# Kernel optimization log

Measured on AMD Instinct MI355X. Metric: run time of the kernel, lower is better.

## Reference

```python
import jax, jax.numpy as jnp
import numpy as np

B, L, ENC_IN, C_OUT = 8, 2048, 21, 21
D_MODEL, EXPAND, D_STATE, D_CONV = 512, 2, 16, 4
D_INNER = D_MODEL * EXPAND
DT_RANK = (D_MODEL + 15) // 16  # 'auto' => ceil(d_model/16) = 32
MARK_DIM = 4  # timeF features for freq='h'
PRED_LEN = 96


def setup_inputs() -> dict:
    key = jax.random.key(0)
    ks = jax.random.split(key, 13)
    s = 0.02
    return {
        'x_enc': jax.random.normal(ks[0], (B, L, ENC_IN), jnp.float32),
        'x_mark_enc': jax.random.normal(ks[1], (B, L, MARK_DIM), jnp.float32),
        'x_dec': jax.random.normal(ks[2], (B, PRED_LEN, ENC_IN), jnp.float32),
        'x_mark_dec': jax.random.normal(ks[3], (B, PRED_LEN, MARK_DIM), jnp.float32),
        'conv_w': jax.random.normal(ks[4], (D_MODEL, ENC_IN, 3), jnp.float32) * s,      # TokenEmbedding circular conv
        'temp_w': jax.random.normal(ks[5], (D_MODEL, MARK_DIM), jnp.float32) * s,       # TimeFeatureEmbedding (no bias)
        'in_proj_w': jax.random.normal(ks[6], (2 * D_INNER, D_MODEL), jnp.float32) * s,
        'conv1d_w': jax.random.normal(ks[7], (D_INNER, 1, D_CONV), jnp.float32) * s,    # depthwise causal conv
        'conv1d_b': jnp.zeros((D_INNER,), jnp.float32),
        'x_proj_w': jax.random.normal(ks[8], (DT_RANK + 2 * D_STATE, D_INNER), jnp.float32) * s,
        'dt_proj_w': jax.random.normal(ks[9], (D_INNER, DT_RANK), jnp.float32) * s,
        'dt_proj_b': jax.random.normal(ks[10], (D_INNER,), jnp.float32) * 0.1,
        'A_log': jnp.log(jnp.tile(jnp.arange(1, D_STATE + 1, dtype=jnp.float32), (D_INNER, 1))),  # mamba S4D-real init
        'D': jnp.ones((D_INNER,), jnp.float32),
        'out_proj_w': jax.random.normal(ks[11], (D_MODEL, D_INNER), jnp.float32) * s,
        'head_w': jax.random.normal(ks[12], (C_OUT, D_MODEL), jnp.float32) * s,
    }


def _pos_embedding(seq_len, d):
    pos = jnp.arange(seq_len, dtype=jnp.float32)[:, None]
    div = jnp.exp(jnp.arange(0, d, 2, dtype=jnp.float32) * (-np.log(10000.0) / d))
    pe = jnp.zeros((seq_len, d), jnp.float32)
    pe = pe.at[:, 0::2].set(jnp.sin(pos * div))
    pe = pe.at[:, 1::2].set(jnp.cos(pos * div))
    return pe


def _mamba(x, in_proj_w, conv1d_w, conv1d_b, x_proj_w, dt_proj_w, dt_proj_b, A_log, D):
    Bsz = x.shape[0]
    xz = x @ in_proj_w.T                          # (B,L,2*Din)
    xs, z = jnp.split(xz, 2, axis=-1)
    # causal depthwise conv1d over time (pad left d_conv-1, truncate to L)
    xc = jnp.pad(xs.transpose(0, 2, 1), ((0, 0), (0, 0), (D_CONV - 1, 0)))
    xc = jax.lax.conv_general_dilated(xc, conv1d_w, (1,), 'VALID',
                                      dimension_numbers=('NCH', 'OIH', 'NCH'),
                                      feature_group_count=D_INNER)
    xs = jax.nn.silu((xc + conv1d_b[None, :, None]).transpose(0, 2, 1))  # (B,L,Din)
    x_dbl = xs @ x_proj_w.T                       # (B,L,dt_rank+2N)
    dt, Bm, Cm = jnp.split(x_dbl, [DT_RANK, DT_RANK + D_STATE], axis=-1)
    delta = jax.nn.softplus(dt @ dt_proj_w.T + dt_proj_b)  # (B,L,Din)
    A = -jnp.exp(A_log)                           # (Din,N)

    def step(h, inp):
        u_t, d_t, b_t, c_t = inp                  # (B,Din),(B,Din),(B,N),(B,N)
        dA = jnp.exp(d_t[:, :, None] * A)         # (B,Din,N)
        h = dA * h + (d_t * u_t)[:, :, None] * b_t[:, None, :]
        return h, jnp.einsum('bdn,bn->bd', h, c_t)

    h0 = jnp.zeros((Bsz, D_INNER, D_STATE), xs.dtype)
    seq = (xs.transpose(1, 0, 2), delta.transpose(1, 0, 2),
           Bm.transpose(1, 0, 2), Cm.transpose(1, 0, 2))
    _, ys = jax.lax.scan(step, h0, seq)
    y = ys.transpose(1, 0, 2) + xs * D            # (B,L,Din)
    return y * jax.nn.silu(z)


def _forward(x_enc, x_mark_enc, conv_w, temp_w, in_proj_w, conv1d_w, conv1d_b,
             x_proj_w, dt_proj_w, dt_proj_b, A_log, D, out_proj_w, head_w):
    # RevIN-style instance norm over time (stats detached)
    mean = jax.lax.stop_gradient(jnp.mean(x_enc, axis=1, keepdims=True))
    xc = x_enc - mean
    std = jax.lax.stop_gradient(jnp.sqrt(jnp.var(xc, axis=1, keepdims=True) + 1e-5))
    xn = xc / std
    # TokenEmbedding: circular-padded conv1d, kernel 3, no bias
    xt = jnp.pad(xn.transpose(0, 2, 1), ((0, 0), (0, 0), (1, 1)), mode='wrap')
    val = jax.lax.conv_general_dilated(xt, conv_w, (1,), 'VALID',
                                       dimension_numbers=('NCH', 'OIH', 'NCH')).transpose(0, 2, 1)
    emb = val + x_mark_enc @ temp_w.T + _pos_embedding(x_enc.shape[1], D_MODEL)[None]
    y = _mamba(emb, in_proj_w, conv1d_w, conv1d_b, x_proj_w, dt_proj_w, dt_proj_b, A_log, D)
    y = y @ out_proj_w.T                          # Mamba out_proj (no bias)
    out = y @ head_w.T                            # final Linear (no bias)
    out = out * std + mean                        # de-normalize
    return out[:, -PRED_LEN:, :]


def reference(x_enc, x_mark_enc, x_dec, x_mark_dec, conv_w, temp_w, in_proj_w,
              conv1d_w, conv1d_b, x_proj_w, dt_proj_w, dt_proj_b, A_log, D,
              out_proj_w, head_w):
    # x_dec / x_mark_dec are accepted but unused by the forecast path
    return _forward(x_enc, x_mark_enc, conv_w, temp_w, in_proj_w, conv1d_w,
                    conv1d_b, x_proj_w, dt_proj_w, dt_proj_b, A_log, D,
                    out_proj_w, head_w)
```

## Files before the change

kernel.cpp:

```cpp
#include <hip/hip_runtime.h>
#include <hip/hip_bf16.h>
#include <math.h>

#define Bsz 8
#define Lseq 2048
#define ENC_IN 21
#define C_OUT 21
#define D_MODEL 512
#define D_INNER 1024
#define D_STATE 16
#define D_CONV 4
#define DT_RANK 32
#define MARK_DIM 4
#define PRED_LEN 96
#define L_TAIL (Lseq - PRED_LEN)
#define K_EMB 80
#define CHUNK 128
#define NCHUNK_A 15
#define MTOT (Bsz * Lseq)
#define PITCH (MTOT + 16)

#define PE_C0 (-9.210340371976184f / (float)D_MODEL)

typedef __attribute__((ext_vector_type(8))) short short8;
typedef __attribute__((ext_vector_type(4))) float f32x4;

__global__ void stats_kernel(const float* __restrict__ x_enc,
                             float* __restrict__ mean, float* __restrict__ stdv) {
    int bc = blockIdx.x;
    int b = bc / ENC_IN, c = bc % ENC_IN;
    __shared__ float red[256], red2[256];
    int t = threadIdx.x;
    float s = 0.f, s2 = 0.f;
    for (int l = t; l < Lseq; l += 256) {
        float x = x_enc[((size_t)b * Lseq + l) * ENC_IN + c];
        s += x; s2 += x * x;
    }
    red[t] = s; red2[t] = s2; __syncthreads();
    for (int off = 128; off > 0; off >>= 1) {
        if (t < off) { red[t] += red[t + off]; red2[t] += red2[t + off]; }
        __syncthreads();
    }
    if (t == 0) {
        float m = red[0] / (float)Lseq;
        float v = red2[0] / (float)Lseq - m * m;
        mean[bc] = m;
        stdv[bc] = sqrtf(fmaxf(v, 0.f) + 1e-5f);
    }
}

__global__ void fuse_w_kernel(const float* __restrict__ head_w,
                              const float* __restrict__ out_proj_w,
                              float* __restrict__ W) {
    int idx = blockIdx.x * 256 + threadIdx.x;
    if (idx >= C_OUT * D_INNER) return;
    int c = idx / D_INNER, d = idx % D_INNER;
    float s = 0.f;
    for (int k = 0; k < D_MODEL; ++k)
        s += head_w[c * D_MODEL + k] * out_proj_w[(size_t)k * D_INNER + d];
    W[idx] = s;
}

__global__ void prep_wT_kernel(const float* __restrict__ conv_w,
                               const float* __restrict__ temp_w,
                               float* __restrict__ WembT) {
    int idx = blockIdx.x * 256 + threadIdx.x;
    int k = idx / D_MODEL, d = idx % D_MODEL;
    float v = 0.f;
    if (k < 3 * ENC_IN) {
        int kk = k / ENC_IN, c = k % ENC_IN;
        v = conv_w[((size_t)d * ENC_IN + c) * 3 + kk];
    } else if (k < 3 * ENC_IN + MARK_DIM) {
        v = temp_w[d * MARK_DIM + (k - 3 * ENC_IN)];
    }
    WembT[idx] = v;
}

__global__ void prep_x_kernel(const float* __restrict__ x_enc,
                              const float* __restrict__ x_mark,
                              const float* __restrict__ mean,
                              const float* __restrict__ stdv,
                              float* __restrict__ xin) {
    int idx = blockIdx.x * 256 + threadIdx.x;
    int bl = idx / K_EMB, k = idx % K_EMB;
    int b = bl >> 11, l = bl & (Lseq - 1);
    float v = 0.f;
    if (k < 3 * ENC_IN) {
        int kk = k / ENC_IN, c = k % ENC_IN;
        int ll = (l + kk - 1 + Lseq) & (Lseq - 1);
        v = (x_enc[((size_t)b * Lseq + ll) * ENC_IN + c] - mean[b * ENC_IN + c])
            / stdv[b * ENC_IN + c];
    } else if (k < 3 * ENC_IN + MARK_DIM) {
        v = x_mark[((size_t)b * Lseq + l) * MARK_DIM + (k - 3 * ENC_IN)];
    }
    xin[idx] = v;
}

__global__ void wcomb_kernel(const float* __restrict__ in_proj_w,
                             const float* __restrict__ WembT,
                             float* __restrict__ Wcomb) {
    int idx = blockIdx.x * 256 + threadIdx.x;
    int j = idx / K_EMB, k = idx % K_EMB;
    const float* a = in_proj_w + (size_t)j * D_MODEL;
    const float* b = WembT + (size_t)k * D_MODEL;
    float s = 0.f;
    for (int d = 0; d < D_MODEL; d += 4) {
        float4 av = *(const float4*)(a + d);
        float4 bv = *(const float4*)(b + d);
        s += av.x * bv.x + av.y * bv.y + av.z * bv.z + av.w * bv.w;
    }
    Wcomb[idx] = s;
}

__global__ void pepz_kernel(const float* __restrict__ in_proj_w,
                            float* __restrict__ PEpZ) {
    __shared__ float per[D_MODEL];
    int lz = blockIdx.x;
    int q = blockIdx.y;
    int t = threadIdx.x;
    {
        int l = L_TAIL + lz;
        float div = __expf((float)(2 * t) * PE_C0);
        float s, c;
        sincosf((float)l * div, &s, &c);
        per[2 * t] = s;
        per[2 * t + 1] = c;
    }
    __syncthreads();
    int j = q * 256 + t;
    const float* w = in_proj_w + (size_t)(D_INNER + j) * D_MODEL;
    float s = 0.f;
    for (int d = 0; d < D_MODEL; d += 4) {
        float4 wv = *(const float4*)(w + d);
        s += per[d] * wv.x + per[d + 1] * wv.y + per[d + 2] * wv.z + per[d + 3] * wv.w;
    }
    PEpZ[(size_t)lz * D_INNER + j] = s;
}

template <int AMODE, int BMODE, int EPI>
__launch_bounds__(256)
__global__ void gemm(const float* __restrict__ A, const float* __restrict__ B,
                     float* __restrict__ C0, const float* __restrict__ bias,
                     int M, int N, int K, int lda, int ldb) {
    __shared__ float As[16][65];
    __shared__ float Bs[16][65];
    int bm = blockIdx.y, bn = blockIdx.x;
    int t = threadIdx.x;
    int tx = t & 15, ty = t >> 4;
    float acc[4][4] = {};
    int arow = bm * 64, bcol = bn * 64;
    int lr = t >> 2;
    int lk = (t & 3) * 4;

    size_t aRow;
    {
        int r = arow + lr;
        if (AMODE == 3) {
            int rb = r / PRED_LEN;
            int rl = r - rb * PRED_LEN;
            aRow = (size_t)rb * Lseq + L_TAIL + rl;
        } else {
            aRow = (size_t)r;
        }
    }

    for (int k0 = 0; k0 < K; k0 += 16) {
        {
            float4 av = *(const float4*)(A + aRow * lda + k0 + lk);
            As[lk + 0][lr] = av.x; As[lk + 1][lr] = av.y;
            As[lk + 2][lr] = av.z; As[lk + 3][lr] = av.w;
        }
        {
            float4 bv = *(const float4*)(B + (size_t)(bcol + lr) * ldb + k0 + lk);
            Bs[lk + 0][lr] = bv.x; Bs[lk + 1][lr] = bv.y;
            Bs[lk + 2][lr] = bv.z; Bs[lk + 3][lr] = bv.w;
        }
        __syncthreads();
        #pragma unroll
        for (int kk = 0; kk < 16; ++kk) {
            float a[4], bq[4];
            #pragma unroll
            for (int i = 0; i < 4; ++i) a[i] = As[kk][ty * 4 + i];
            #pragma unroll
            for (int j = 0; j < 4; ++j) bq[j] = Bs[kk][tx * 4 + j];
            #pragma unroll
            for (int i = 0; i < 4; ++i)
                #pragma unroll
                for (int j = 0; j < 4; ++j)
                    acc[i][j] += a[i] * bq[j];
        }
        __syncthreads();
    }

    #pragma unroll
    for (int i = 0; i < 4; ++i) {
        int row = arow + ty * 4 + i;
        #pragma unroll
        for (int j = 0; j < 4; ++j) {
            int col = bcol + tx * 4 + j;
            float v = acc[i][j];
            if (EPI == 3) {
                v += bias[(size_t)(row % PRED_LEN) * N + col];
            }
            C0[(size_t)row * N + col] = v;
        }
    }
}

__device__ __forceinline__ void split_bf16(float x, short& hb, short& lb) {
    unsigned u = __float_as_uint(x);
    unsigned short h = (unsigned short)(u >> 16);
    float hf = __uint_as_float(((unsigned)h) << 16);
    unsigned short l = (unsigned short)(__float_as_uint(x - hf) >> 16);
    hb = (short)h; lb = (short)l;
}

template <int BMODE, int EPI>
__launch_bounds__(256)
__global__ void mfma_gemm128(const float* __restrict__ A, const float* __restrict__ B,
                             float* __restrict__ C, const float* __restrict__ bias,
                             int M, int N, int K, int lda, int ldb, int ldc) {
    __shared__ short Ah[128][48], Al[128][48];
    __shared__ short Bh[64][48], Bl[64][48];
    int t = threadIdx.x;
    int bn0 = blockIdx.x * 64;
    int am0 = blockIdx.y * 128;
    int w = t >> 6, l = t & 63;
    int lr = l & 15, lk = l >> 4;

    f32x4 acc[2][4];
    #pragma unroll
    for (int i = 0; i < 2; ++i)
        #pragma unroll
        for (int j = 0; j < 4; ++j) acc[i][j] = (f32x4){0.f, 0.f, 0.f, 0.f};

    const int mst = t >> 2, kst = (t & 3) * 8;

    for (int kb = 0; kb < K; kb += 32) {
        if (kb) __syncthreads();
        #pragma unroll
        for (int half = 0; half < 2; ++half) {
            int m = mst + half * 64;
            const float* src = A + (size_t)(am0 + m) * lda + kb + kst;
            short8 hv, lv;
            if (kb + 32 <= K) {
                float4 a0 = *(const float4*)(src);
                float4 a1 = *(const float4*)(src + 4);
                float xs[8] = {a0.x, a0.y, a0.z, a0.w, a1.x, a1.y, a1.z, a1.w};
                #pragma unroll
                for (int j = 0; j < 8; ++j) {
                    short hb, lb; split_bf16(xs[j], hb, lb);
                    hv[j] = hb; lv[j] = lb;
                }
            } else {
                #pragma unroll
                for (int j = 0; j < 8; ++j) {
                    float x = (kb + kst + j < K) ? src[j] : 0.f;
                    short hb, lb; split_bf16(x, hb, lb);
                    hv[j] = hb; lv[j] = lb;
                }
            }
            *(short8*)&Ah[m][kst] = hv;
            *(short8*)&Al[m][kst] = lv;
        }
        if constexpr (BMODE == 0) {
            short8 hv, lv;
            #pragma unroll
            for (int j = 0; j < 8; ++j) {
                int k = kb + kst + j;
                float x = (k < K) ? B[(size_t)k * ldb + bn0 + mst] : 0.f;
                short hb, lb; split_bf16(x, hb, lb);
                hv[j] = hb; lv[j] = lb;
            }
            *(short8*)&Bh[mst][kst] = hv;
            *(short8*)&Bl[mst][kst] = lv;
        } else if constexpr (BMODE == 1) {
            float ng = (float)(bn0 + mst);
            short8 hv, lv;
            #pragma unroll
            for (int p = 0; p < 4; ++p) {
                float e = __expf((float)(kb + kst + 2 * p) * PE_C0);
                float sv, cv;
                sincosf(ng * e, &sv, &cv);
                short hb, lb;
                split_bf16(sv, hb, lb); hv[2 * p] = hb; lv[2 * p] = lb;
                split_bf16(cv, hb, lb); hv[2 * p + 1] = hb; lv[2 * p + 1] = lb;
            }
            *(short8*)&Bh[mst][kst] = hv;
            *(short8*)&Bl[mst][kst] = lv;
        } else {
            const float* src = B + (size_t)(bn0 + mst) * ldb + kb + kst;
            short8 hv, lv;
            if (kb + 32 <= K) {
                float4 b0 = *(const float4*)(src);
                float4 b1 = *(const float4*)(src + 4);
                float xs[8] = {b0.x, b0.y, b0.z, b0.w, b1.x, b1.y, b1.z, b1.w};
                #pragma unroll
                for (int j = 0; j < 8; ++j) {
                    short hb, lb; split_bf16(xs[j], hb, lb);
                    hv[j] = hb; lv[j] = lb;
                }
            } else {
                #pragma unroll
                for (int j = 0; j < 8; ++j) {
                    float x = (kb + kst + j < K) ? src[j] : 0.f;
                    short hb, lb; split_bf16(x, hb, lb);
                    hv[j] = hb; lv[j] = lb;
                }
            }
            *(short8*)&Bh[mst][kst] = hv;
            *(short8*)&Bl[mst][kst] = lv;
        }
        __syncthreads();
        #pragma unroll
        for (int mt = 0; mt < 2; ++mt) {
            short8 a_hi = *(const short8*)&Ah[mt * 64 + w * 16 + lr][lk * 8];
            short8 a_lo = *(const short8*)&Al[mt * 64 + w * 16 + lr][lk * 8];
            #pragma unroll
            for (int t4 = 0; t4 < 4; ++t4) {
                short8 b_hi = *(const short8*)&Bh[t4 * 16 + lr][lk * 8];
                short8 b_lo = *(const short8*)&Bl[t4 * 16 + lr][lk * 8];
                acc[mt][t4] = __builtin_amdgcn_mfma_f32_16x16x32_bf16(a_hi, b_hi, acc[mt][t4], 0, 0, 0);
                acc[mt][t4] = __builtin_amdgcn_mfma_f32_16x16x32_bf16(a_lo, b_hi, acc[mt][t4], 0, 0, 0);
                acc[mt][t4] = __builtin_amdgcn_mfma_f32_16x16x32_bf16(a_hi, b_lo, acc[mt][t4], 0, 0, 0);
            }
        }
    }

    #pragma unroll
    for (int mt = 0; mt < 2; ++mt) {
        #pragma unroll
        for (int t4 = 0; t4 < 4; ++t4) {
            #pragma unroll
            for (int r = 0; r < 4; ++r) {
                int row = am0 + mt * 64 + w * 16 + lk * 4 + r;
                int col = bn0 + t4 * 16 + lr;
                float v = acc[mt][t4][r];
                if (EPI == 1) {
                    v += bias[row];
                    v = (v > 20.f) ? v : log1pf(__expf(v));
                }
                if (EPI == 2) {
                    v += bias[(size_t)row * Lseq + (col & (Lseq - 1))];
                }
                C[(size_t)row * ldc + col] = v;
            }
        }
    }
}

template <int BMODE, int EPI>
__launch_bounds__(256)
__global__ void mfma_gemm64(const float* __restrict__ A, const float* __restrict__ B,
                            float* __restrict__ C, const float* __restrict__ bias,
                            int M, int N, int K, int lda, int ldb, int ldc) {
    __shared__ short Ah[64][48], Al[64][48];
    __shared__ short Bh[64][48], Bl[64][48];
    int t = threadIdx.x;
    int bn0 = blockIdx.x * 64;
    int am0 = blockIdx.y * 64;
    int w = t >> 6, l = t & 63;
    int lr = l & 15, lk = l >> 4;

    f32x4 acc[4];
    #pragma unroll
    for (int i = 0; i < 4; ++i) acc[i] = (f32x4){0.f, 0.f, 0.f, 0.f};

    const int mst = t >> 2, kst = (t & 3) * 8;

    for (int kb = 0; kb < K; kb += 32) {
        if (kb) __syncthreads();
        {
            const float* src = A + (size_t)(am0 + mst) * lda + kb + kst;
            short8 hv, lv;
            if (kb + 32 <= K) {
                float4 a0 = *(const float4*)(src);
                float4 a1 = *(const float4*)(src + 4);
                float xs[8] = {a0.x, a0.y, a0.z, a0.w, a1.x, a1.y, a1.z, a1.w};
                #pragma unroll
                for (int j = 0; j < 8; ++j) {
                    short hb, lb; split_bf16(xs[j], hb, lb);
                    hv[j] = hb; lv[j] = lb;
                }
            } else {
                #pragma unroll
                for (int j = 0; j < 8; ++j) {
                    float x = (kb + kst + j < K) ? src[j] : 0.f;
                    short hb, lb; split_bf16(x, hb, lb);
                    hv[j] = hb; lv[j] = lb;
                }
            }
            *(short8*)&Ah[mst][kst] = hv;
            *(short8*)&Al[mst][kst] = lv;
        }
        if constexpr (BMODE == 1) {
            float ng = (float)(bn0 + mst);
            short8 hv, lv;
            #pragma unroll
            for (int p = 0; p < 4; ++p) {
                float e = __expf((float)(kb + kst + 2 * p) * PE_C0);
                float sv, cv;
                sincosf(ng * e, &sv, &cv);
                short hb, lb;
                split_bf16(sv, hb, lb); hv[2 * p] = hb; lv[2 * p] = lb;
                split_bf16(cv, hb, lb); hv[2 * p + 1] = hb; lv[2 * p + 1] = lb;
            }
            *(short8*)&Bh[mst][kst] = hv;
            *(short8*)&Bl[mst][kst] = lv;
        } else {
            short8 hv, lv;
            #pragma unroll
            for (int j = 0; j < 8; ++j) {
                int k = kb + kst + j;
                float x = (k < K) ? B[(size_t)k * ldb + bn0 + mst] : 0.f;
                short hb, lb; split_bf16(x, hb, lb);
                hv[j] = hb; lv[j] = lb;
            }
            *(short8*)&Bh[mst][kst] = hv;
            *(short8*)&Bl[mst][kst] = lv;
        }
        __syncthreads();
        short8 a_hi = *(const short8*)&Ah[w * 16 + lr][lk * 8];
        short8 a_lo = *(const short8*)&Al[w * 16 + lr][lk * 8];
        #pragma unroll
        for (int t4 = 0; t4 < 4; ++t4) {
            short8 b_hi = *(const short8*)&Bh[t4 * 16 + lr][lk * 8];
            short8 b_lo = *(const short8*)&Bl[t4 * 16 + lr][lk * 8];
            acc[t4] = __builtin_amdgcn_mfma_f32_16x16x32_bf16(a_hi, b_hi, acc[t4], 0, 0, 0);
            acc[t4] = __builtin_amdgcn_mfma_f32_16x16x32_bf16(a_lo, b_hi, acc[t4], 0, 0, 0);
            acc[t4] = __builtin_amdgcn_mfma_f32_16x16x32_bf16(a_hi, b_lo, acc[t4], 0, 0, 0);
        }
    }

    #pragma unroll
    for (int t4 = 0; t4 < 4; ++t4) {
        #pragma unroll
        for (int r = 0; r < 4; ++r) {
            int row = am0 + w * 16 + lk * 4 + r;
            int col = bn0 + t4 * 16 + lr;
            C[(size_t)row * ldc + col] = acc[t4][r];
        }
    }
}

__launch_bounds__(256)
__global__ void mfma_gemm_splitk(const float* __restrict__ A, const float* __restrict__ B,
                                 float* __restrict__ C,
                                 int M, int N, int K, int lda, int ldb, int ldc,
                                 int ksplit) {
    __shared__ short Ah[64][48], Al[64][48];
    __shared__ short Bh[64][48], Bl[64][48];
    int t = threadIdx.x;
    int bn0 = blockIdx.x * 64;
    int kz0 = blockIdx.z * ksplit;
    int kz1 = min(K, kz0 + ksplit);
    int w = t >> 6, l = t & 63;
    int lr = l & 15, lk = l >> 4;

    f32x4 acc[4];
    #pragma unroll
    for (int i = 0; i < 4; ++i) acc[i] = (f32x4){0.f, 0.f, 0.f, 0.f};

    const int mst = t >> 2, kst = (t & 3) * 8;

    for (int kb = kz0; kb < kz1; kb += 32) {
        if (kb != kz0) __syncthreads();
        {
            const float* src = A + (size_t)mst * lda + kb + kst;
            float4 a0 = *(const float4*)(src);
            float4 a1 = *(const float4*)(src + 4);
            float xs[8] = {a0.x, a0.y, a0.z, a0.w, a1.x, a1.y, a1.z, a1.w};
            short8 hv, lv;
            #pragma unroll
            for (int j = 0; j < 8; ++j) {
                short hb, lb; split_bf16(xs[j], hb, lb);
                hv[j] = hb; lv[j] = lb;
            }
            *(short8*)&Ah[mst][kst] = hv;
            *(short8*)&Al[mst][kst] = lv;
        }
        {
            short8 hv, lv;
            #pragma unroll
            for (int j = 0; j < 8; ++j) {
                int k = kb + kst + j;
                float x = B[(size_t)k * ldb + bn0 + mst];
                short hb, lb; split_bf16(x, hb, lb);
                hv[j] = hb; lv[j] = lb;
            }
            *(short8*)&Bh[mst][kst] = hv;
            *(short8*)&Bl[mst][kst] = lv;
        }
        __syncthreads();
        short8 a_hi = *(const short8*)&Ah[w * 16 + lr][lk * 8];
        short8 a_lo = *(const short8*)&Al[w * 16 + lr][lk * 8];
        #pragma unroll
        for (int t4 = 0; t4 < 4; ++t4) {
            short8 b_hi = *(const short8*)&Bh[t4 * 16 + lr][lk * 8];
            short8 b_lo = *(const short8*)&Bl[t4 * 16 + lr][lk * 8];
            acc[t4] = __builtin_amdgcn_mfma_f32_16x16x32_bf16(a_hi, b_hi, acc[t4], 0, 0, 0);
            acc[t4] = __builtin_amdgcn_mfma_f32_16x16x32_bf16(a_lo, b_hi, acc[t4], 0, 0, 0);
            acc[t4] = __builtin_amdgcn_mfma_f32_16x16x32_bf16(a_hi, b_lo, acc[t4], 0, 0, 0);
        }
    }

    #pragma unroll
    for (int t4 = 0; t4 < 4; ++t4) {
        #pragma unroll
        for (int r = 0; r < 4; ++r) {
            int row = w * 16 + lk * 4 + r;
            int col = bn0 + t4 * 16 + lr;
            atomicAdd(&C[(size_t)row * ldc + col], acc[t4][r]);
        }
    }
}

__global__ void zero_kernel(float4* __restrict__ p) {
    p[(size_t)blockIdx.x * 256 + threadIdx.x] = make_float4(0.f, 0.f, 0.f, 0.f);
}

__global__ void xdbl_tr_kernel(const float* __restrict__ xdblT,
                               float* __restrict__ xdbl_rm) {
    __shared__ float tile[32][65];
    int l0 = blockIdx.x * 64;
    int t = threadIdx.x;
    {
        int p = t >> 3, ls = (t & 7) * 8;
        const float* src = xdblT + (size_t)p * PITCH + l0 + ls;
        float4 v0 = *(const float4*)(src);
        float4 v1 = *(const float4*)(src + 4);
        tile[p][ls + 0] = v0.x; tile[p][ls + 1] = v0.y;
        tile[p][ls + 2] = v0.z; tile[p][ls + 3] = v0.w;
        tile[p][ls + 4] = v1.x; tile[p][ls + 5] = v1.y;
        tile[p][ls + 6] = v1.z; tile[p][ls + 7] = v1.w;
    }
    __syncthreads();
    {
        int ll = t >> 2, ps = (t & 3) * 8;
        float o[8];
        #pragma unroll
        for (int j = 0; j < 8; ++j) o[j] = tile[ps + j][ll];
        float* dst = xdbl_rm + (size_t)(l0 + ll) * DT_RANK + ps;
        *(float4*)(dst)     = make_float4(o[0], o[1], o[2], o[3]);
        *(float4*)(dst + 4) = make_float4(o[4], o[5], o[6], o[7]);
    }
}

__global__ void dwconv_kernel(const float* __restrict__ xs_rawT,
                              const float* __restrict__ w,
                              const float* __restrict__ bias,
                              float* __restrict__ outT) {
    int bid = blockIdx.x;
    int d = bid & (D_INNER - 1), ch = bid >> 10;
    int t = threadIdx.x;
    int lbase = ch * 1024 + t * 4;
    const float* row = xs_rawT + (size_t)d * MTOT;
    float w0 = w[d * D_CONV + 0], w1 = w[d * D_CONV + 1];
    float w2 = w[d * D_CONV + 2], w3 = w[d * D_CONV + 3];
    float bs = bias[d];
    float4 cur = *(const float4*)(row + lbase);
    float4 pv = make_float4(0.f, 0.f, 0.f, 0.f);
    if (lbase >= 4) pv = *(const float4*)(row + lbase - 4);
    float v[7] = {pv.y, pv.z, pv.w, cur.x, cur.y, cur.z, cur.w};
    int lpos = lbase & (Lseq - 1);
    float o[4];
    if (lpos != 0) {
        #pragma unroll
        for (int j = 0; j < 4; ++j)
            o[j] = bs + w0 * v[j] + w1 * v[j + 1] + w2 * v[j + 2] + w3 * v[j + 3];
    } else {
        #pragma unroll
        for (int j = 0; j < 4; ++j) {
            float acc = bs;
            #pragma unroll
            for (int k2 = 0; k2 < 4; ++k2) {
                int ll = j - 3 + k2;
                if (ll >= 0) acc += v[j + k2] * ((k2 == 0) ? w0 : (k2 == 1) ? w1 : (k2 == 2) ? w2 : w3);
            }
            o[j] = acc;
        }
    }
    float4 res;
    res.x = o[0] / (1.f + __expf(-o[0]));
    res.y = o[1] / (1.f + __expf(-o[1]));
    res.z = o[2] / (1.f + __expf(-o[2]));
    res.w = o[3] / (1.f + __expf(-o[3]));
    *(float4*)(outT + (size_t)d * PITCH + lbase) = res;
}

__launch_bounds__(256, 4)
__global__ void scanA_kernel(const float* __restrict__ deltaT,
                             const float* __restrict__ uT,
                             const float* __restrict__ xdblT,
                             const float* __restrict__ A_log,
                             float* __restrict__ Pa,
                             float* __restrict__ Sa) {
    int b = blockIdx.x >> 4;
    int dg = blockIdx.x & 15;
    int c = blockIdx.y;
    int t = threadIdx.x;
    int dgrp = t >> 4, n = t & 15;
    int d0 = dg * 64 + dgrp;

    float A[4], P[4], S[4];
    const float *pd[4], *pu[4];
    #pragma unroll
    for (int vd = 0; vd < 4; ++vd) {
        int d = d0 + 16 * vd;
        A[vd] = -__expf(A_log[d * D_STATE + n]);
        P[vd] = 1.f; S[vd] = 0.f;
        size_t base = (size_t)d * PITCH + b * Lseq + c * CHUNK;
        pd[vd] = deltaT + base;
        pu[vd] = uT + base;
    }
    const float* pB = xdblT + (size_t)(DT_RANK + n) * PITCH + b * Lseq + c * CHUNK;

    const int NI = CHUNK / 4;
    float4 BvA, dvA[4], uvA[4];
    float4 BvB, dvB[4], uvB[4];

    BvA = *(const float4*)(pB);
    #pragma unroll
    for (int vd = 0; vd < 4; ++vd) {
        dvA[vd] = *(const float4*)(pd[vd]);
        uvA[vd] = *(const float4*)(pu[vd]);
    }

    for (int i = 0; i < NI; i += 2) {
        BvB = *(const float4*)(pB + 4 * (i + 1));
        #pragma unroll
        for (int vd = 0; vd < 4; ++vd) {
            dvB[vd] = *(const float4*)(pd[vd] + 4 * (i + 1));
            uvB[vd] = *(const float4*)(pu[vd] + 4 * (i + 1));
        }
        #pragma unroll
        for (int vd = 0; vd < 4; ++vd) {
            float a;
            a = __expf(dvA[vd].x * A[vd]); P[vd] *= a; S[vd] = a * S[vd] + (dvA[vd].x * uvA[vd].x) * BvA.x;
            a = __expf(dvA[vd].y * A[vd]); P[vd] *= a; S[vd] = a * S[vd] + (dvA[vd].y * uvA[vd].y) * BvA.y;
            a = __expf(dvA[vd].z * A[vd]); P[vd] *= a; S[vd] = a * S[vd] + (dvA[vd].z * uvA[vd].z) * BvA.z;
            a = __expf(dvA[vd].w * A[vd]); P[vd] *= a; S[vd] = a * S[vd] + (dvA[vd].w * uvA[vd].w) * BvA.w;
        }
        int i2 = (i + 2 < NI) ? (i + 2) : (NI - 1);
        BvA = *(const float4*)(pB + 4 * i2);
        #pragma unroll
        for (int vd = 0; vd < 4; ++vd) {
            dvA[vd] = *(const float4*)(pd[vd] + 4 * i2);
            uvA[vd] = *(const float4*)(pu[vd] + 4 * i2);
        }
        #pragma unroll
        for (int vd = 0; vd < 4; ++vd) {
            float a;
            a = __expf(dvB[vd].x * A[vd]); P[vd] *= a; S[vd] = a * S[vd] + (dvB[vd].x * uvB[vd].x) * BvB.x;
            a = __expf(dvB[vd].y * A[vd]); P[vd] *= a; S[vd] = a * S[vd] + (dvB[vd].y * uvB[vd].y) * BvB.y;
            a = __expf(dvB[vd].z * A[vd]); P[vd] *= a; S[vd] = a * S[vd] + (dvB[vd].z * uvB[vd].z) * BvB.z;
            a = __expf(dvB[vd].w * A[vd]); P[vd] *= a; S[vd] = a * S[vd] + (dvB[vd].w * uvB[vd].w) * BvB.w;
        }
    }
    #pragma unroll
    for (int vd = 0; vd < 4; ++vd) {
        int d = d0 + 16 * vd;
        size_t o = ((size_t)(b * NCHUNK_A + c) * D_INNER + d) * 16 + n;
        Pa[o] = P[vd];
        Sa[o] = S[vd];
    }
}

__launch_bounds__(256)
__global__ void scanB_kernel(const float* __restrict__ deltaT,
                             const float* __restrict__ uT,
                             const float* __restrict__ xdblT,
                             const float* __restrict__ A_log,
                             const float* __restrict__ Dp,
                             const float* __restrict__ Pa,
                             const float* __restrict__ Sa,
                             const float* __restrict__ z96,
                             float* __restrict__ y96) {
    int b = blockIdx.x >> 6;
    int dg = blockIdx.x & 63;
    int t = threadIdx.x;
    int d = dg * 16 + (t >> 4);
    int n = t & 15;
    float A = -__expf(A_log[d * D_STATE + n]);
    float Dd = Dp[d];
    float h = 0.f;
    for (int c = 0; c < NCHUNK_A; ++c) {
        size_t o = ((size_t)(b * NCHUNK_A + c) * D_INNER + d) * 16 + n;
        h = Pa[o] * h + Sa[o];
    }
    const int lt0 = NCHUNK_A * CHUNK;
    size_t base = (size_t)d * PITCH + b * Lseq + lt0;
    const float* pd = deltaT + base;
    const float* pu = uT + base;
    const float* pB = xdblT + (size_t)(DT_RANK + n) * PITCH + b * Lseq + lt0;
    const float* pC = xdblT + (size_t)(DT_RANK + D_STATE + n) * PITCH + b * Lseq + lt0;

    #pragma unroll 2
    for (int i = 0; i < 8; ++i) {
        float4 dv = *(const float4*)(pd + 4 * i);
        float4 uv = *(const float4*)(pu + 4 * i);
        float4 Bv = *(const float4*)(pB + 4 * i);
        float a;
        a = __expf(dv.x * A); h = a * h + (dv.x * uv.x) * Bv.x;
        a = __expf(dv.y * A); h = a * h + (dv.y * uv.y) * Bv.y;
        a = __expf(dv.z * A); h = a * h + (dv.z * uv.z) * Bv.z;
        a = __expf(dv.w * A); h = a * h + (dv.w * uv.w) * Bv.w;
    }
    for (int i = 8; i < 32; ++i) {
        float4 dv = *(const float4*)(pd + 4 * i);
        float4 uv = *(const float4*)(pu + 4 * i);
        float4 Bv = *(const float4*)(pB + 4 * i);
        float4 Cv = *(const float4*)(pC + 4 * i);
        #pragma unroll
        for (int j = 0; j < 4; ++j) {
            float dl = (j == 0) ? dv.x : (j == 1) ? dv.y : (j == 2) ? dv.z : dv.w;
            float uu = (j == 0) ? uv.x : (j == 1) ? uv.y : (j == 2) ? uv.z : uv.w;
            float Bb = (j == 0) ? Bv.x : (j == 1) ? Bv.y : (j == 2) ? Bv.z : Bv.w;
            float Cc = (j == 0) ? Cv.x : (j == 1) ? Cv.y : (j == 2) ? Cv.z : Cv.w;
            float a = __expf(dl * A);
            h = a * h + (dl * uu) * Bb;
            float y = h * Cc;
            #pragma unroll
            for (int m = 8; m >= 1; m >>= 1) y += __shfl_xor(y, m, 16);
            if (n == 0) {
                int lz = (lt0 + 4 * i + j) - L_TAIL;
                size_t o = ((size_t)b * PRED_LEN + lz) * D_INNER + d;
                float z = z96[o];
                y96[o] = (y + uu * Dd) * (z / (1.f + __expf(-z)));
            }
        }
    }
}

__global__ void head_kernel(const float* __restrict__ y96,
                            const float* __restrict__ W,
                            const float* __restrict__ mean,
                            const float* __restrict__ stdv,
                            float* __restrict__ out) {
    int idx = blockIdx.x;
    int c = idx % C_OUT;
    int bt = idx / C_OUT;
    int b = bt / PRED_LEN;
    int lane = threadIdx.x;
    const float* yrow = y96 + (size_t)bt * D_INNER;
    const float* wrow = W + (size_t)c * D_INNER;
    float s = 0.f;
    for (int d = lane; d < D_INNER; d += 64) s += yrow[d] * wrow[d];
    #pragma unroll
    for (int m = 32; m >= 1; m >>= 1) s += __shfl_xor(s, m, 64);
    if (lane == 0)
        out[(size_t)bt * C_OUT + c] = s * stdv[b * C_OUT + c] + mean[b * C_OUT + c];
}

extern "C" void kernel_launch(void* const* d_in, const int* in_sizes, int n_in,
                              void* d_out, int out_size, void* d_ws, size_t ws_size,
                              hipStream_t stream) {
    const float* x_enc     = (const float*)d_in[0];
    const float* x_mark    = (const float*)d_in[1];
    const float* conv_w    = (const float*)d_in[4];
    const float* temp_w    = (const float*)d_in[5];
    const float* in_proj_w = (const float*)d_in[6];
    const float* conv1d_w  = (const float*)d_in[7];
    const float* conv1d_b  = (const float*)d_in[8];
    const float* x_proj_w  = (const float*)d_in[9];
    const float* dt_proj_w = (const float*)d_in[10];
    const float* dt_proj_b = (const float*)d_in[11];
    const float* A_log     = (const float*)d_in[12];
    const float* Dp        = (const float*)d_in[13];
    const float* out_proj_w= (const float*)d_in[14];
    const float* head_w    = (const float*)d_in[15];
    float* out = (float*)d_out;
    float* ws = (float*)d_ws;

    size_t off = 0;
    float* mean     = ws + off; off += 256;
    float* stdv     = ws + off; off += 256;
    float* W        = ws + off; off += (size_t)C_OUT * D_INNER;
    float* WembT    = ws + off; off += (size_t)K_EMB * D_MODEL;
    float* Wcomb    = ws + off; off += (size_t)2 * D_INNER * K_EMB;
    float* PEpT     = ws + off; off += (size_t)D_INNER * Lseq;
    float* PEpZ     = ws + off; off += (size_t)PRED_LEN * D_INNER;
    float* xin      = ws + off; off += (size_t)K_EMB * MTOT;
    float* xs_rawT  = ws + off; off += (size_t)D_INNER * MTOT;
    float* z96      = ws + off; off += (size_t)Bsz * PRED_LEN * D_INNER;
    float* xs_convT = ws + off; off += (size_t)D_INNER * PITCH;
    float* xdblT    = ws + off; off += (size_t)64 * PITCH;
    float* deltaT   = ws + off; off += (size_t)D_INNER * PITCH;
    float* Pa       = ws + off; off += (size_t)Bsz * NCHUNK_A * D_INNER * D_STATE;
    float* Sa       = ws + off; off += (size_t)Bsz * NCHUNK_A * D_INNER * D_STATE;
    float* y96      = ws + off; off += (size_t)Bsz * PRED_LEN * D_INNER;
    float* xdbl_rm  = ws + off; off += (size_t)MTOT * DT_RANK;

    stats_kernel<<<Bsz * ENC_IN, 256, 0, stream>>>(x_enc, mean, stdv);
    fuse_w_kernel<<<(C_OUT * D_INNER + 255) / 256, 256, 0, stream>>>(head_w, out_proj_w, W);
    prep_wT_kernel<<<(K_EMB * D_MODEL) / 256, 256, 0, stream>>>(conv_w, temp_w, WembT);
    prep_x_kernel<<<(MTOT * K_EMB) / 256, 256, 0, stream>>>(x_enc, x_mark, mean, stdv, xin);
    wcomb_kernel<<<(2 * D_INNER * K_EMB) / 256, 256, 0, stream>>>(in_proj_w, WembT, Wcomb);
    pepz_kernel<<<dim3(PRED_LEN, 4), 256, 0, stream>>>(in_proj_w, PEpZ);
    mfma_gemm64<1, 0><<<dim3(Lseq / 64, D_INNER / 64), 256, 0, stream>>>(
        in_proj_w, nullptr, PEpT, nullptr, D_INNER, Lseq, D_MODEL, D_MODEL, 0, Lseq);
    mfma_gemm128<2, 2><<<dim3(MTOT / 64, D_INNER / 128), 256, 0, stream>>>(
        Wcomb, xin, xs_rawT, PEpT, D_INNER, MTOT, K_EMB, K_EMB, K_EMB, MTOT);
    gemm<3, 0, 3><<<dim3(D_INNER / 64, (Bsz * PRED_LEN) / 64), 256, 0, stream>>>(
        xin, Wcomb + (size_t)D_INNER * K_EMB, z96, PEpZ,
        Bsz * PRED_LEN, D_INNER, K_EMB, K_EMB, K_EMB);
    dwconv_kernel<<<D_INNER * 16, 256, 0, stream>>>(xs_rawT, conv1d_w, conv1d_b, xs_convT);
    zero_kernel<<<(64 * PITCH) / 4 / 256, 256, 0, stream>>>((float4*)xdblT);
    mfma_gemm_splitk<<<dim3(MTOT / 64, 1, 4), 256, 0, stream>>>(
        x_proj_w, xs_convT, xdblT, 64, MTOT, D_INNER, D_INNER, PITCH, PITCH, 256);
    xdbl_tr_kernel<<<MTOT / 64, 256, 0, stream>>>(xdblT, xdbl_rm);
    mfma_gemm128<2, 1><<<dim3(MTOT / 64, D_INNER / 128), 256, 0, stream>>>(
        dt_proj_w, xdbl_rm, deltaT, dt_proj_b, D_INNER, MTOT, DT_RANK, DT_RANK, DT_RANK, PITCH);
    scanA_kernel<<<dim3(Bsz * 16, NCHUNK_A), 256, 0, stream>>>(
        deltaT, xs_convT, xdblT, A_log, Pa, Sa);
    scanB_kernel<<<Bsz * 64, 256, 0, stream>>>(
        deltaT, xs_convT, xdblT, A_log, Dp, Pa, Sa, z96, y96);
    head_kernel<<<Bsz * PRED_LEN * C_OUT, 64, 0, stream>>>(y96, W, mean, stdv, out);
}
```

Before: 456.9 us.

## Fuse depthwise causal conv and SiLU into in_proj GEMM epilogue

The xs in_proj GEMM now stages its output tile in shared memory, recomputes the three preceding columns as halo with scalar dot products, and applies the depthwise causal conv plus SiLU before writing xs_convT directly. This removes the separate dwconv kernel and the round trip of the 1024xMTOT raw activation buffer through global memory. In exchange each block does extra scalar halo work and an extra shared-memory pass, and the shared buffer is aliased between operand tiles and the output tile.

```diff
diff --git a/kernel.cpp b/kernel.cpp
--- a/kernel.cpp
+++ b/kernel.cpp
@@ -219,9 +219,15 @@
 __launch_bounds__(256)
 __global__ void mfma_gemm128(const float* __restrict__ A, const float* __restrict__ B,
                              float* __restrict__ C, const float* __restrict__ bias,
+                             const float* __restrict__ cw, const float* __restrict__ cb,
                              int M, int N, int K, int lda, int ldb, int ldc) {
-    __shared__ short Ah[128][48], Al[128][48];
-    __shared__ short Bh[64][48], Bl[64][48];
+    __shared__ __align__(16) char smem[36864];
+    short (*Ah)[48] = (short(*)[48])(smem);
+    short (*Al)[48] = (short(*)[48])(smem + 12288);
+    short (*Bh)[48] = (short(*)[48])(smem + 24576);
+    short (*Bl)[48] = (short(*)[48])(smem + 30720);
+    float (*tile)[68] = (float(*)[68])(smem);
+
     int t = threadIdx.x;
     int bn0 = blockIdx.x * 64;
     int am0 = blockIdx.y * 128;
@@ -327,23 +333,80 @@
         }
     }
 
-    #pragma unroll
-    for (int mt = 0; mt < 2; ++mt) {
-        #pragma unroll
-        for (int t4 = 0; t4 < 4; ++t4) {
+    if constexpr (EPI == 3) {
+        __syncthreads();
+        #pragma unroll
+        for (int mt = 0; mt < 2; ++mt) {
+            #pragma unroll
+            for (int t4 = 0; t4 < 4; ++t4) {
+                #pragma unroll
+                for (int r = 0; r < 4; ++r) {
+                    int rl = mt * 64 + w * 16 + lk * 4 + r;
+                    int cl = t4 * 16 + lr;
+                    int col = bn0 + cl;
+                    tile[rl][3 + cl] = acc[mt][t4][r]
+                        + bias[(size_t)(am0 + rl) * Lseq + (col & (Lseq - 1))];
+                }
+            }
+        }
+        for (int idx = t; idx < 384; idx += 256) {
+            int rl = idx / 3;
+            int dlt = idx % 3 + 1;
+            float val = 0.f;
+            if ((bn0 & (Lseq - 1)) != 0) {
+                int col = bn0 - dlt;
+                const float* ar = A + (size_t)(am0 + rl) * lda;
+                const float* br = B + (size_t)col * ldb;
+                float s = 0.f;
+                for (int k = 0; k < K; k += 4) {
+                    float4 a4 = *(const float4*)(ar + k);
+                    float4 b4 = *(const float4*)(br + k);
+                    s += a4.x * b4.x + a4.y * b4.y + a4.z * b4.z + a4.w * b4.w;
+                }
+                val = s + bias[(size_t)(am0 + rl) * Lseq + (col & (Lseq - 1))];
+            }
+            tile[rl][3 - dlt] = val;
+        }
+        __syncthreads();
+        #pragma unroll
+        for (int mt = 0; mt < 2; ++mt) {
             #pragma unroll
             for (int r = 0; r < 4; ++r) {
-                int row = am0 + mt * 64 + w * 16 + lk * 4 + r;
-                int col = bn0 + t4 * 16 + lr;
-                float v = acc[mt][t4][r];
-                if (EPI == 1) {
-                    v += bias[row];
-                    v = (v > 20.f) ? v : log1pf(__expf(v));
-                }
-                if (EPI == 2) {
-                    v += bias[(size_t)row * Lseq + (col & (Lseq - 1))];
-                }
-                C[(size_t)row * ldc + col] = v;
+                int rl = mt * 64 + w * 16 + lk * 4 + r;
+                int d = am0 + rl;
+                float w0 = cw[d * D_CONV + 0], w1 = cw[d * D_CONV + 1];
+                float w2 = cw[d * D_CONV + 2], w3 = cw[d * D_CONV + 3];
+                float bs = cb[d];
+                #pragma unroll
+                for (int t4 = 0; t4 < 4; ++t4) {
+                    int cl = t4 * 16 + lr;
+                    float x0 = tile[rl][cl], x1 = tile[rl][cl + 1];
+                    float x2 = tile[rl][cl + 2], x3 = tile[rl][cl + 3];
+                    float o = bs + w0 * x0 + w1 * x1 + w2 * x2 + w3 * x3;
+                    o = o / (1.f + __expf(-o));
+                    C[(size_t)d * ldc + bn0 + cl] = o;
+                }
+            }
+        }
+    } else {
+        #pragma unroll
+        for (int mt = 0; mt < 2; ++mt) {
+            #pragma unroll
+            for (int t4 = 0; t4 < 4; ++t4) {
+                #pragma unroll
+                for (int r = 0; r < 4; ++r) {
+                    int row = am0 + mt * 64 + w * 16 + lk * 4 + r;
+                    int col = bn0 + t4 * 16 + lr;
+                    float v = acc[mt][t4][r];
+                    if (EPI == 1) {
+                        v += bias[row];
+                        v = (v > 20.f) ? v : log1pf(__expf(v));
+                    }
+                    if (EPI == 2) {
+                        v += bias[(size_t)row * Lseq + (col & (Lseq - 1))];
+                    }
+                    C[(size_t)row * ldc + col] = v;
+                }
             }
         }
     }
@@ -544,48 +607,6 @@
         *(float4*)(dst)     = make_float4(o[0], o[1], o[2], o[3]);
         *(float4*)(dst + 4) = make_float4(o[4], o[5], o[6], o[7]);
     }
-}
-
-__global__ void dwconv_kernel(const float* __restrict__ xs_rawT,
-                              const float* __restrict__ w,
-                              const float* __restrict__ bias,
-                              float* __restrict__ outT) {
-    int bid = blockIdx.x;
-    int d = bid & (D_INNER - 1), ch = bid >> 10;
-    int t = threadIdx.x;
-    int lbase = ch * 1024 + t * 4;
-    const float* row = xs_rawT + (size_t)d * MTOT;
-    float w0 = w[d * D_CONV + 0], w1 = w[d * D_CONV + 1];
-    float w2 = w[d * D_CONV + 2], w3 = w[d * D_CONV + 3];
-    float bs = bias[d];
-    float4 cur = *(const float4*)(row + lbase);
-    float4 pv = make_float4(0.f, 0.f, 0.f, 0.f);
-    if (lbase >= 4) pv = *(const float4*)(row + lbase - 4);
-    float v[7] = {pv.y, pv.z, pv.w, cur.x, cur.y, cur.z, cur.w};
-    int lpos = lbase & (Lseq - 1);
-    float o[4];
-    if (lpos != 0) {
-        #pragma unroll
-        for (int j = 0; j < 4; ++j)
-            o[j] = bs + w0 * v[j] + w1 * v[j + 1] + w2 * v[j + 2] + w3 * v[j + 3];
-    } else {
-        #pragma unroll
-        for (int j = 0; j < 4; ++j) {
-            float acc = bs;
-            #pragma unroll
-            for (int k2 = 0; k2 < 4; ++k2) {
-                int ll = j - 3 + k2;
-                if (ll >= 0) acc += v[j + k2] * ((k2 == 0) ? w0 : (k2 == 1) ? w1 : (k2 == 2) ? w2 : w3);
-            }
-            o[j] = acc;
-        }
-    }
-    float4 res;
-    res.x = o[0] / (1.f + __expf(-o[0]));
-    res.y = o[1] / (1.f + __expf(-o[1]));
-    res.z = o[2] / (1.f + __expf(-o[2]));
-    res.w = o[3] / (1.f + __expf(-o[3]));
-    *(float4*)(outT + (size_t)d * PITCH + lbase) = res;
 }
 
 __launch_bounds__(256, 4)
@@ -781,7 +802,6 @@
     float* PEpT     = ws + off; off += (size_t)D_INNER * Lseq;
     float* PEpZ     = ws + off; off += (size_t)PRED_LEN * D_INNER;
     float* xin      = ws + off; off += (size_t)K_EMB * MTOT;
-    float* xs_rawT  = ws + off; off += (size_t)D_INNER * MTOT;
     float* z96      = ws + off; off += (size_t)Bsz * PRED_LEN * D_INNER;
     float* xs_convT = ws + off; off += (size_t)D_INNER * PITCH;
     float* xdblT    = ws + off; off += (size_t)64 * PITCH;
@@ -799,18 +819,19 @@
     pepz_kernel<<<dim3(PRED_LEN, 4), 256, 0, stream>>>(in_proj_w, PEpZ);
     mfma_gemm64<1, 0><<<dim3(Lseq / 64, D_INNER / 64), 256, 0, stream>>>(
         in_proj_w, nullptr, PEpT, nullptr, D_INNER, Lseq, D_MODEL, D_MODEL, 0, Lseq);
-    mfma_gemm128<2, 2><<<dim3(MTOT / 64, D_INNER / 128), 256, 0, stream>>>(
-        Wcomb, xin, xs_rawT, PEpT, D_INNER, MTOT, K_EMB, K_EMB, K_EMB, MTOT);
+    mfma_gemm128<2, 3><<<dim3(MTOT / 64, D_INNER / 128), 256, 0, stream>>>(
+        Wcomb, xin, xs_convT, PEpT, conv1d_w, conv1d_b,
+        D_INNER, MTOT, K_EMB, K_EMB, K_EMB, PITCH);
     gemm<3, 0, 3><<<dim3(D_INNER / 64, (Bsz * PRED_LEN) / 64), 256, 0, stream>>>(
         xin, Wcomb + (size_t)D_INNER * K_EMB, z96, PEpZ,
         Bsz * PRED_LEN, D_INNER, K_EMB, K_EMB, K_EMB);
-    dwconv_kernel<<<D_INNER * 16, 256, 0, stream>>>(xs_rawT, conv1d_w, conv1d_b, xs_convT);
     zero_kernel<<<(64 * PITCH) / 4 / 256, 256, 0, stream>>>((float4*)xdblT);
     mfma_gemm_splitk<<<dim3(MTOT / 64, 1, 4), 256, 0, stream>>>(
         x_proj_w, xs_convT, xdblT, 64, MTOT, D_INNER, D_INNER, PITCH, PITCH, 256);
     xdbl_tr_kernel<<<MTOT / 64, 256, 0, stream>>>(xdblT, xdbl_rm);
     mfma_gemm128<2, 1><<<dim3(MTOT / 64, D_INNER / 128), 256, 0, stream>>>(
-        dt_proj_w, xdbl_rm, deltaT, dt_proj_b, D_INNER, MTOT, DT_RANK, DT_RANK, DT_RANK, PITCH);
+        dt_proj_w, xdbl_rm, deltaT, dt_proj_b, nullptr, nullptr,
+        D_INNER, MTOT, DT_RANK, DT_RANK, DT_RANK, PITCH);
     scanA_kernel<<<dim3(Bsz * 16, NCHUNK_A), 256, 0, stream>>>(
         deltaT, xs_convT, xdblT, A_log, Pa, Sa);
     scanB_kernel<<<Bsz * 64, 256, 0, stream>>>(
```

After: 462.0 us. No clear change (+1.1%).
